# Performance work log

Measured on AMD Instinct MI355X. Metric: run time of the kernel, lower is better.

The kernel has to match this reference:

```python
import jax, jax.numpy as jnp
from jax import lax
import numpy as np

EPS = 1e-5
K = 3


def _conv(x, w, b, pad, dil=1, groups=1):
    out = lax.conv_general_dilated(
        x, w, (1, 1), [(pad, pad), (pad, pad)], rhs_dilation=(dil, dil),
        dimension_numbers=('NCHW', 'OIHW', 'NCHW'), feature_group_count=groups)
    return out + b[None, :, None, None]


def _bn(x, g, b, m, v):
    scale = g / jnp.sqrt(v + EPS)
    return (x - m[None, :, None, None]) * scale[None, :, None, None] + b[None, :, None, None]


def setup_inputs() -> dict:
    key = jax.random.key(0)
    ks = jax.random.split(key, 24)
    B, C, H, W = 8, 256, 48, 80
    Hd = 256  # hidden_channels
    n = lambda k, s, sc=0.05: (jax.random.normal(k, s, dtype=jnp.float32) * sc)
    return {
        'f_t_minus_2': jax.random.normal(ks[0], (B, C, H, W), dtype=jnp.float32),
        'f_t_minus_1': jax.random.normal(ks[1], (B, C, H, W), dtype=jnp.float32),
        'f_t':         jax.random.normal(ks[2], (B, C, H, W), dtype=jnp.float32),
        'ov_w1': n(ks[3], (Hd, 3 * C, 3, 3)), 'ov_b1': n(ks[4], (Hd,)),
        'bn1_g': jnp.ones((Hd,), jnp.float32), 'bn1_b': jnp.zeros((Hd,), jnp.float32),
        'bn1_m': n(ks[5], (Hd,)), 'bn1_v': jax.random.uniform(ks[6], (Hd,), jnp.float32, 0.5, 1.5),
        'ov_w2': n(ks[7], (Hd, Hd, 3, 3)), 'ov_b2': n(ks[8], (Hd,)),
        'bn2_g': jnp.ones((Hd,), jnp.float32), 'bn2_b': jnp.zeros((Hd,), jnp.float32),
        'bn2_m': n(ks[9], (Hd,)), 'bn2_v': jax.random.uniform(ks[10], (Hd,), jnp.float32, 0.5, 1.5),
        'g_w': n(ks[11], (C, Hd, 1, 1)), 'g_b': n(ks[12], (C,)),
        'fc1_w': n(ks[13], (512, 2 * C)), 'fc1_b': n(ks[14], (512,)),
        'fc2_w': n(ks[15], (C * K * K, 512)), 'fc2_b': n(ks[16], (C * K * K,)),
        'ap_w': n(ks[17], (1, 2 * C, 1, 1)), 'ap_b': n(ks[18], (1,)),
        'a_w': n(ks[19], (1, 2 * C, 1, 1)), 'a_b': jnp.ones((1,), jnp.float32),
    }


def reference(f_t_minus_2, f_t_minus_1, f_t,
              ov_w1, ov_b1, bn1_g, bn1_b, bn1_m, bn1_v,
              ov_w2, ov_b2, bn2_g, bn2_b, bn2_m, bn2_v,
              g_w, g_b, fc1_w, fc1_b, fc2_w, fc2_b,
              ap_w, ap_b, a_w, a_b):
    B, C, H, W = f_t.shape
    # (1) Overview-Net (GCM)
    f_concat = jnp.concatenate([f_t_minus_2, f_t_minus_1, f_t], axis=1)
    h = jax.nn.relu(_bn(_conv(f_concat, ov_w1, ov_b1, pad=2, dil=2), bn1_g, bn1_b, bn1_m, bn1_v))
    h = jax.nn.relu(_bn(_conv(h, ov_w2, ov_b2, pad=4, dil=4), bn2_g, bn2_b, bn2_m, bn2_v))
    g_pooled = h.mean(axis=(2, 3), keepdims=True)            # [B,Hd,1,1]
    G = _conv(g_pooled, g_w, g_b, pad=0)                     # [B,C,1,1]
    # (2) Focus-Net: FC-generated per-(batch,channel) 3x3 depthwise conv on (f_t, f_{t-1})
    Fs = jnp.concatenate([f_t, f_t_minus_1], axis=0)         # [2B,C,H,W]
    g_flat = jnp.repeat(G.reshape(B, C), 2, axis=0)          # [2B,C]
    gap = Fs.mean(axis=(2, 3))                               # [2B,C]
    fc_in = jnp.concatenate([g_flat, gap], axis=1)           # [2B,2C]
    w = jax.nn.silu(fc_in @ fc1_w.T + fc1_b) @ fc2_w.T + fc2_b  # [2B, C*9]
    w = w.reshape(2 * B * C, 1, K, K)
    x = Fs.reshape(1, 2 * B * C, H, W)
    out = lax.conv_general_dilated(
        x, w, (1, 1), [(1, 1), (1, 1)],
        dimension_numbers=('NCHW', 'OIHW', 'NCHW'), feature_group_count=2 * B * C)
    out = out.reshape(2 * B, C, H, W)
    f_t_mod, f_t1_mod = out[:B], out[B:]
    # (3) Dynamic fusion
    f_prev_cat = jnp.concatenate([f_t1_mod, f_t_minus_2], axis=1)
    alpha_prev = 0.3 + 0.4 * jax.nn.sigmoid(_conv(f_prev_cat, ap_w, ap_b, pad=0))
    f_prev = alpha_prev * f_t1_mod + (1.0 - alpha_prev) * f_t_minus_2
    f_cat = jnp.concatenate([f_t_mod, f_prev], axis=1)
    alpha = 0.6 + 0.3 * jax.nn.sigmoid(_conv(f_cat, a_w, a_b, pad=0))
    return alpha * f_t_mod + (1.0 - alpha) * f_prev
```

## Files before the change

kernel.cpp:

```cpp
#include <hip/hip_runtime.h>
#include <hip/hip_bf16.h>
#include <math.h>


typedef __bf16 bf16x8 __attribute__((ext_vector_type(8)));
typedef float f32x4 __attribute__((ext_vector_type(4)));
typedef __attribute__((address_space(1))) void as1_void;
typedef __attribute__((address_space(3))) void as3_void;

__global__ __launch_bounds__(256) void aux_kernel(
    const float* __restrict__ w1, const float* __restrict__ w2,
    const float* __restrict__ ob1, const float* __restrict__ g1, const float* __restrict__ b1,
    const float* __restrict__ m1, const float* __restrict__ v1,
    const float* __restrict__ ob2, const float* __restrict__ g2, const float* __restrict__ b2,
    const float* __restrict__ m2, const float* __restrict__ v2,
    __hip_bfloat16* __restrict__ wt1, __hip_bfloat16* __restrict__ wt2,
    __hip_bfloat16* __restrict__ h1p, float* __restrict__ gzero,
    float* __restrict__ cst)
{
  __shared__ float wl[1152];
  const int bid = blockIdx.x;
  const uint4 z4 = {0u, 0u, 0u, 0u};

  if (bid < 2048) {
    const float* w = (bid < 1536) ? w1 : w2;
    __hip_bfloat16* out = (bid < 1536) ? wt1 : wt2;
    const int IC = (bid < 1536) ? 768 : 256;
    const int lb = (bid < 1536) ? bid : (bid - 1536);
    const int nicb = IC >> 7;
    const int icb = lb % nicb, oc = lb / nicb;
    const int ic0 = icb * 128;
    const float* src = w + ((size_t)oc * IC + ic0) * 9;
    for (int k = threadIdx.x; k < 1152; k += 256) wl[k] = src[k];
    __syncthreads();
    if (threadIdx.x < 144) {
      const int tap = threadIdx.x / 16, ch = threadIdx.x % 16;
      union { __hip_bfloat16 h[8]; uint4 u; } pk;
#pragma unroll
      for (int j = 0; j < 8; j++) pk.h[j] = __float2bfloat16(wl[(ch * 8 + j) * 9 + tap]);
      *(uint4*)(out + ((size_t)tap * 256 + oc) * IC + ic0 + ch * 8) = pk.u;
    }
  } else if (bid < 3136) {
    const int s = (bid - 2048) * 256 + threadIdx.x;
    const int px = s >> 5, ch8 = s & 31;
    const int b = px / 1088, r = px % 1088;
    int y, x;
    if (r < 704) { const int yi = r / 88; y = (yi < 4) ? yi : 48 + yi; x = r % 88; }
    else { const int r2 = r - 704; y = 4 + (r2 >> 3); const int xi = r2 & 7; x = (xi < 4) ? xi : 80 + xi; }
    *(uint4*)(h1p + ((size_t)(b * 56 + y) * 88 + x) * 256 + ch8 * 8) = z4;
  } else if (bid < 3142) {
    ((uint4*)gzero)[(bid - 3136) * 256 + threadIdx.x] = z4;
  } else {
    const int i = threadIdx.x;
    float a1 = g1[i] / sqrtf(v1[i] + 1e-5f);
    cst[i]       = a1;
    cst[256 + i] = (ob1[i] - m1[i]) * a1 + b1[i];
    float a2 = g2[i] / sqrtf(v2[i] + 1e-5f);
    cst[512 + i] = a2;
    cst[768 + i] = (ob2[i] - m2[i]) * a2 + b2[i];
  }
}

__global__ __launch_bounds__(256) void pad_concat_kernel(
    const float* __restrict__ f2, const float* __restrict__ f1, const float* __restrict__ f0,
    __hip_bfloat16* __restrict__ out, float* __restrict__ gapv)
{
  int bid = blockIdx.x;
  const int cg = bid % 6; bid /= 6;
  const int y = bid % 48;
  const int b = bid / 48;

  __shared__ float tile[128 * 85];

  const float* src = (cg < 2) ? f2 : ((cg < 4) ? f1 : f0);
  const int ccbase = (cg & 1) * 128;
  const uint4 z4 = {0u, 0u, 0u, 0u};

#pragma unroll
  for (int it = 0; it < 10; it++) {
    const int idx = it * 256 + threadIdx.x;
    const int cl = idx / 20, x4 = idx % 20;
    const float4 v = *(const float4*)(src +
        (((size_t)b * 256 + ccbase + cl) * 48 + y) * 80 + x4 * 4);
    float* t = tile + cl * 85 + x4 * 4;
    t[0] = v.x; t[1] = v.y; t[2] = v.z; t[3] = v.w;
  }

  if (threadIdx.x < 32) {
    const int xb_ = threadIdx.x >> 3, ch8 = threadIdx.x & 7;
    const int xx = (xb_ < 2) ? xb_ : (80 + xb_);
    *(uint4*)(out + ((size_t)(b * 52 + y + 2) * 84 + xx) * 768 + cg * 128 + ch8 * 8) = z4;
  }
  if (y == 0 || y == 47) {
    const int r0 = (y == 0) ? 0 : 50;
    for (int idx = threadIdx.x; idx < 1344; idx += 256) {
      const int rr = idx / 672, rem = idx % 672;
      const int xx = rem >> 3, ch8 = rem & 7;
      *(uint4*)(out + ((size_t)(b * 52 + r0 + rr) * 84 + xx) * 768 + cg * 128 + ch8 * 8) = z4;
    }
  }
  __syncthreads();

  __hip_bfloat16* obase = out + ((size_t)(b * 52 + y + 2) * 84 + 2) * 768 + cg * 128;
#pragma unroll
  for (int it = 0; it < 5; it++) {
    const int idx = it * 256 + threadIdx.x;
    const int chunk = idx & 15, x = idx >> 4;
    const float* t = tile + chunk * 8 * 85 + x;
    union { __hip_bfloat16 h[8]; uint4 u; } pk;
#pragma unroll
    for (int j = 0; j < 8; j++) pk.h[j] = __float2bfloat16(t[j * 85]);
    *(uint4*)(obase + (size_t)x * 768 + chunk * 8) = pk.u;
  }

  if (cg >= 2) {
    const int i_gap = (cg >= 4) ? b : (b + 8);
    const int cl = threadIdx.x >> 1, half = threadIdx.x & 1;
    const float* t = tile + cl * 85 + half * 40;
    float s = 0.f;
#pragma unroll
    for (int k = 0; k < 40; k++) s += t[k];
    s += __shfl_xor(s, 1);
    if (half == 0) atomicAdd(&gapv[i_gap * 256 + ccbase + cl], s);
  }
}

template <int CIN, int HP, int WP, int DIL, int MODE>
__global__ __launch_bounds__(256) void conv_mfma_kernel(
    const __hip_bfloat16* __restrict__ inp, const __hip_bfloat16* __restrict__ wt,
    const float* __restrict__ bnA, const float* __restrict__ bnB,
    __hip_bfloat16* __restrict__ outp, float* __restrict__ gpool)
{
  __shared__ unsigned short As[8192] __attribute__((aligned(16)));
  __shared__ unsigned short Bs[8192] __attribute__((aligned(16)));

  int bid = blockIdx.x;
  bid = (bid & 7) * 60 + (bid >> 3);
  const int ocb = bid & 1; bid >>= 1;
  const int xb = bid % 5; bid /= 5;
  const int yb = bid % 6; bid /= 6;
  const int b = bid;
  const int y0 = yb * 8, x0 = xb * 16, oc0 = ocb * 128;

  const int t = threadIdx.x;
  const int w = t >> 6, l = t & 63;
  const int col16 = l & 15, quad = l >> 4;
  const int wm = w >> 1, wn = w & 1;
  const int rsub = l >> 3;
  const int jj = (l & 7) ^ rsub;

  f32x4 acc[4][4];
  const f32x4 zf = {0.f, 0.f, 0.f, 0.f};
#pragma unroll
  for (int i = 0; i < 4; i++)
#pragma unroll
    for (int j = 0; j < 4; j++) acc[i][j] = zf;

  for (int c0 = 0; c0 < CIN; c0 += 64) {
    for (int tap = 0; tap < 9; tap++) {
      const int ty = tap / 3, tx = tap - ty * 3;
      const __hip_bfloat16* inBase =
          inp + ((size_t)(b * HP + y0 + DIL * ty) * WP + (x0 + DIL * tx)) * CIN + jj * 8 + c0;
      const __hip_bfloat16* wBase = wt + (size_t)(tap * 256 + oc0) * CIN + jj * 8 + c0;
      __syncthreads();
#pragma unroll
      for (int i = 0; i < 4; i++) {
        const int q = i * 4 + w;
        const int m = q * 8 + rsub;
        const int ry = m >> 4, rx = m & 15;
        const __hip_bfloat16* gp = inBase + (ry * WP + rx) * CIN;
        __builtin_amdgcn_global_load_lds((as1_void*)gp,
            (as3_void*)((char*)As + q * 1024), 16, 0, 0);
      }
#pragma unroll
      for (int i = 0; i < 4; i++) {
        const int q = i * 4 + w;
        const int n = q * 8 + rsub;
        const __hip_bfloat16* gp = wBase + n * CIN;
        __builtin_amdgcn_global_load_lds((as1_void*)gp,
            (as3_void*)((char*)Bs + q * 1024), 16, 0, 0);
      }
      __syncthreads();
#pragma unroll
      for (int kiter = 0; kiter < 2; kiter++) {
        bf16x8 af[4], bg[4];
#pragma unroll
        for (int fi = 0; fi < 4; fi++) {
          const int m = wm * 64 + fi * 16 + col16;
          const int jc = (kiter * 4 + quad) ^ (m & 7);
          af[fi] = *(const bf16x8*)((const char*)As + m * 128 + jc * 16);
        }
#pragma unroll
        for (int fi = 0; fi < 4; fi++) {
          const int n = wn * 64 + fi * 16 + col16;
          const int jc = (kiter * 4 + quad) ^ (n & 7);
          bg[fi] = *(const bf16x8*)((const char*)Bs + n * 128 + jc * 16);
        }
#pragma unroll
        for (int fm_ = 0; fm_ < 4; fm_++)
#pragma unroll
          for (int fn_ = 0; fn_ < 4; fn_++)
            acc[fm_][fn_] = __builtin_amdgcn_mfma_f32_16x16x32_bf16(
                af[fm_], bg[fn_], acc[fm_][fn_], 0, 0, 0);
      }
    }
  }

  if (MODE == 0) {
#pragma unroll
    for (int fn_ = 0; fn_ < 4; fn_++) {
      const int oc = oc0 + wn * 64 + fn_ * 16 + col16;
      const float sa = bnA[oc], sb = bnB[oc];
#pragma unroll
      for (int fm_ = 0; fm_ < 4; fm_++) {
#pragma unroll
        for (int r = 0; r < 4; r++) {
          const int m = wm * 64 + fm_ * 16 + quad * 4 + r;
          const int y = y0 + (m >> 4), x = x0 + (m & 15);
          const float v = fmaxf(acc[fm_][fn_][r] * sa + sb, 0.f);
          outp[((size_t)(b * 56 + y + 4) * 88 + (x + 4)) * 256 + oc] = __float2bfloat16(v);
        }
      }
    }
  } else {
#pragma unroll
    for (int fn_ = 0; fn_ < 4; fn_++) {
      const int oc = oc0 + wn * 64 + fn_ * 16 + col16;
      const float sa = bnA[oc], sb = bnB[oc];
      float cs = 0.f;
#pragma unroll
      for (int fm_ = 0; fm_ < 4; fm_++)
#pragma unroll
        for (int r = 0; r < 4; r++)
          cs += fmaxf(acc[fm_][fn_][r] * sa + sb, 0.f);
      cs += __shfl_xor(cs, 16);
      cs += __shfl_xor(cs, 32);
      if (quad == 0) atomicAdd(&gpool[b * 256 + oc], cs);
    }
  }
}


__global__ __launch_bounds__(256) void fcG_kernel(
    const float* __restrict__ gpool, const float* __restrict__ gw,
    const float* __restrict__ gb, float* __restrict__ G)
{
  int b = blockIdx.x, oc = threadIdx.x;
  __shared__ float pool[256];
  pool[oc] = gpool[b * 256 + oc] * (1.f / 3840.f);
  __syncthreads();
  float s = gb[oc];
  const float* wr = gw + oc * 256;
  for (int c2 = 0; c2 < 256; c2++) s += pool[c2] * wr[c2];
  G[b * 256 + oc] = s;
}

__global__ __launch_bounds__(256) void fc1_kernel(
    const float* __restrict__ G, const float* __restrict__ gapv,
    const float* __restrict__ w, const float* __restrict__ bias,
    float* __restrict__ out1)
{
  __shared__ float fin[16][513];
  for (int idx = threadIdx.x; idx < 16 * 512; idx += 256) {
    int i = idx >> 9, k = idx & 511;
    fin[i][k] = (k < 256) ? G[(i >> 1) * 256 + k]
                          : gapv[i * 256 + (k - 256)] * (1.f / 3840.f);
  }
  __syncthreads();
  int g = blockIdx.x * 256 + threadIdx.x;
  int j = g >> 4, i = g & 15;
  float s = bias[j];
  const float* wr = w + j * 512;
  for (int k = 0; k < 512; k++) s += fin[i][k] * wr[k];
  out1[j * 16 + i] = s / (1.f + expf(-s));
}

__global__ __launch_bounds__(256) void fc2_kernel(
    const float* __restrict__ out1, const float* __restrict__ w,
    const float* __restrict__ bias, float* __restrict__ wdw)
{
  __shared__ float fin[16][513];
  for (int idx = threadIdx.x; idx < 16 * 512; idx += 256) {
    int i = idx >> 9, k = idx & 511;
    fin[i][k] = out1[k * 16 + i];
  }
  __syncthreads();
  int g = blockIdx.x * 256 + threadIdx.x;
  int j = g >> 4, i = g & 15;
  float s = bias[j];
  const float* wr = w + j * 512;
  for (int k = 0; k < 512; k++) s += fin[i][k] * wr[k];
  wdw[i * 2304 + j] = s;
}

__global__ __launch_bounds__(256) void dw_kernel(
    const float* __restrict__ f0, const float* __restrict__ f1,
    const float* __restrict__ wdw, float* __restrict__ fm)
{
  int i = blockIdx.x >> 8, c = blockIdx.x & 255;
  const float* src = (i < 8) ? (f0 + ((size_t)i * 256 + c) * 3840)
                             : (f1 + ((size_t)(i - 8) * 256 + c) * 3840);
  float* dst = fm + ((size_t)i * 256 + c) * 3840;
  __shared__ float w9s[9];
  __shared__ float tile[50][82];
  for (int k = threadIdx.x; k < 4100; k += 256) ((float*)tile)[k] = 0.f;
  if (threadIdx.x < 9) w9s[threadIdx.x] = wdw[i * 2304 + c * 9 + threadIdx.x];
  __syncthreads();
  for (int k = threadIdx.x; k < 960; k += 256) {
    const float4 v = *(const float4*)(src + k * 4);
    const int y = k / 20, xx = (k % 20) * 4;
    float* tp = &tile[y + 1][xx + 1];
    tp[0] = v.x; tp[1] = v.y; tp[2] = v.z; tp[3] = v.w;
  }
  __syncthreads();
  for (int k = threadIdx.x; k < 960; k += 256) {
    const int y = k / 20, xx = (k % 20) * 4;
    float r0 = 0.f, r1 = 0.f, r2 = 0.f, r3 = 0.f;
#pragma unroll
    for (int dy = 0; dy < 3; dy++) {
      const float* row = &tile[y + dy][xx];
      const float w0 = w9s[dy * 3], w1 = w9s[dy * 3 + 1], w2 = w9s[dy * 3 + 2];
      r0 += w0 * row[0] + w1 * row[1] + w2 * row[2];
      r1 += w0 * row[1] + w1 * row[2] + w2 * row[3];
      r2 += w0 * row[2] + w1 * row[3] + w2 * row[4];
      r3 += w0 * row[3] + w1 * row[4] + w2 * row[5];
    }
    float4 o; o.x = r0; o.y = r1; o.z = r2; o.w = r3;
    *(float4*)(dst + k * 4) = o;
  }
}

__global__ __launch_bounds__(640) void alpha_final_kernel(
    const float* __restrict__ fm, const float* __restrict__ f2,
    const float* __restrict__ apw, const float* __restrict__ apb,
    const float* __restrict__ aw, const float* __restrict__ ab,
    float* __restrict__ out)
{
  int b = blockIdx.x / 48, y = blockIdx.x % 48;
  int x = threadIdx.x % 80, g = threadIdx.x / 80;
  const float* ftm  = fm + ((size_t)(b * 256) + g * 32) * 3840 + y * 80 + x;
  const float* ft1m = fm + ((size_t)((b + 8) * 256) + g * 32) * 3840 + y * 80 + x;
  const float* ptm2 = f2 + ((size_t)(b * 256) + g * 32) * 3840 + y * 80 + x;

  float v0[32], v1[32], v2[32];
  float S = 0.f, T0 = 0.f, T1 = 0.f, T2 = 0.f;
#pragma unroll
  for (int cc = 0; cc < 32; cc++) {
    v0[cc] = ftm[(size_t)cc * 3840];
    v1[cc] = ft1m[(size_t)cc * 3840];
    v2[cc] = ptm2[(size_t)cc * 3840];
    const int c = g * 32 + cc;
    S  += apw[c] * v1[cc] + apw[256 + c] * v2[cc];
    T0 += aw[c] * v0[cc];
    T1 += aw[256 + c] * v1[cc];
    T2 += aw[256 + c] * v2[cc];
  }
  __shared__ float red[4][8][80];
  __shared__ float apl[80], alb[80];
  red[0][g][x] = S; red[1][g][x] = T0; red[2][g][x] = T1; red[3][g][x] = T2;
  __syncthreads();
  if (g == 0) {
    float s = 0.f, t0 = 0.f, t1 = 0.f, t2 = 0.f;
#pragma unroll
    for (int k = 0; k < 8; k++) {
      s += red[0][k][x]; t0 += red[1][k][x]; t1 += red[2][k][x]; t2 += red[3][k][x];
    }
    float ap = 0.3f + 0.4f / (1.f + expf(-(s + apb[0])));
    float A  = t0 + ap * t1 + (1.f - ap) * t2 + ab[0];
    float al = 0.6f + 0.3f / (1.f + expf(-A));
    apl[x] = ap; alb[x] = al;
  }
  __syncthreads();
  const float ap = apl[x], al = alb[x];
  float* ob = out + ((size_t)(b * 256) + g * 32) * 3840 + y * 80 + x;
#pragma unroll
  for (int cc = 0; cc < 32; cc++)
    ob[(size_t)cc * 3840] = al * v0[cc] + (1.f - al) * (ap * v1[cc] + (1.f - ap) * v2[cc]);
}


extern "C" void kernel_launch(void* const* d_in, const int* in_sizes, int n_in,
                              void* d_out, int out_size, void* d_ws, size_t ws_size,
                              hipStream_t stream)
{
  const float* f_tm2 = (const float*)d_in[0];
  const float* f_tm1 = (const float*)d_in[1];
  const float* f_t   = (const float*)d_in[2];
  const float* ov_w1 = (const float*)d_in[3];
  const float* ov_b1 = (const float*)d_in[4];
  const float* bn1_g = (const float*)d_in[5];
  const float* bn1_b = (const float*)d_in[6];
  const float* bn1_m = (const float*)d_in[7];
  const float* bn1_v = (const float*)d_in[8];
  const float* ov_w2 = (const float*)d_in[9];
  const float* ov_b2 = (const float*)d_in[10];
  const float* bn2_g = (const float*)d_in[11];
  const float* bn2_b = (const float*)d_in[12];
  const float* bn2_m = (const float*)d_in[13];
  const float* bn2_v = (const float*)d_in[14];
  const float* g_w   = (const float*)d_in[15];
  const float* g_b   = (const float*)d_in[16];
  const float* fc1_w = (const float*)d_in[17];
  const float* fc1_b = (const float*)d_in[18];
  const float* fc2_w = (const float*)d_in[19];
  const float* fc2_b = (const float*)d_in[20];
  const float* ap_w  = (const float*)d_in[21];
  const float* ap_b  = (const float*)d_in[22];
  const float* a_w   = (const float*)d_in[23];
  const float* a_b   = (const float*)d_in[24];

  char* ws = (char*)d_ws;
  float* fm            = (float*)ws;
  __hip_bfloat16* in1p = (__hip_bfloat16*)ws;
  __hip_bfloat16* wt1  = (__hip_bfloat16*)(ws + 53673984);
  __hip_bfloat16* wt2  = (__hip_bfloat16*)(ws + 57212928);
  __hip_bfloat16* h1p  = (__hip_bfloat16*)(ws + 58392576);
  float* gpool         = (float*)(ws + 78577664);
  float* gapv          = (float*)(ws + 78585856);
  float* Gv            = (float*)(ws + 78602240);
  float* out1          = (float*)(ws + 78610432);
  float* wdw           = (float*)(ws + 78643200);
  float* cst           = (float*)(ws + 79036416);

  aux_kernel<<<3143, 256, 0, stream>>>(ov_w1, ov_w2,
      ov_b1, bn1_g, bn1_b, bn1_m, bn1_v, ov_b2, bn2_g, bn2_b, bn2_m, bn2_v,
      wt1, wt2, h1p, gpool, cst);
  pad_concat_kernel<<<2304, 256, 0, stream>>>(f_tm2, f_tm1, f_t, in1p, gapv);

  conv_mfma_kernel<768, 52, 84, 2, 0><<<480, 256, 0, stream>>>(in1p, wt1, cst, cst + 256, h1p, nullptr);
  conv_mfma_kernel<256, 56, 88, 4, 1><<<480, 256, 0, stream>>>(h1p, wt2, cst + 512, cst + 768, nullptr, gpool);

  fcG_kernel<<<8, 256, 0, stream>>>(gpool, g_w, g_b, Gv);
  fc1_kernel<<<32, 256, 0, stream>>>(Gv, gapv, fc1_w, fc1_b, out1);
  fc2_kernel<<<144, 256, 0, stream>>>(out1, fc2_w, fc2_b, wdw);
  dw_kernel<<<4096, 256, 0, stream>>>(f_t, f_tm1, wdw, fm);
  alpha_final_kernel<<<384, 640, 0, stream>>>(fm, f_tm2, ap_w, ap_b, a_w, a_b, (float*)d_out);
}
```

Before: 444.6 us.

## Merge prep kernels, fold fcG into fc1, vectorize alpha-final with float4

Merges the pad/concat kernel and the auxiliary weight/pad/BN-constant kernel into a single prep launch, and zeroes gpool and gapv with one hipMemsetAsync instead of the zeroing blocks. The fcG matvec is folded into fc1, with each of the 32 blocks recomputing G redundantly so one launch and one global round-trip go away. The final alpha blend kernel now uses float4 loads and stores over 8 channels per thread, with a four-stage shared-memory reduction. The aim is to cut launch overhead and widen memory accesses, at the cost of repeated fcG work and more barriers in the reduction.

```diff
diff --git a/kernel.cpp b/kernel.cpp
--- a/kernel.cpp
+++ b/kernel.cpp
@@ -8,48 +8,112 @@
 typedef __attribute__((address_space(1))) void as1_void;
 typedef __attribute__((address_space(3))) void as3_void;
 
-__global__ __launch_bounds__(256) void aux_kernel(
+__device__ __forceinline__ void f4acc(float4& a, float s, const float4& v) {
+  a.x += s * v.x; a.y += s * v.y; a.z += s * v.z; a.w += s * v.w;
+}
+__device__ __forceinline__ float blend1(float al, float ap, float a, float b, float c) {
+  return al * a + (1.f - al) * (ap * b + (1.f - ap) * c);
+}
+
+__global__ __launch_bounds__(256) void prep_kernel(
+    const float* __restrict__ f2, const float* __restrict__ f1, const float* __restrict__ f0,
+    __hip_bfloat16* __restrict__ out, float* __restrict__ gapv,
     const float* __restrict__ w1, const float* __restrict__ w2,
     const float* __restrict__ ob1, const float* __restrict__ g1, const float* __restrict__ b1,
     const float* __restrict__ m1, const float* __restrict__ v1,
     const float* __restrict__ ob2, const float* __restrict__ g2, const float* __restrict__ b2,
     const float* __restrict__ m2, const float* __restrict__ v2,
     __hip_bfloat16* __restrict__ wt1, __hip_bfloat16* __restrict__ wt2,
-    __hip_bfloat16* __restrict__ h1p, float* __restrict__ gzero,
-    float* __restrict__ cst)
-{
-  __shared__ float wl[1152];
-  const int bid = blockIdx.x;
+    __hip_bfloat16* __restrict__ h1p, float* __restrict__ cst)
+{
+  __shared__ float shbuf[128 * 85];
   const uint4 z4 = {0u, 0u, 0u, 0u};
 
-  if (bid < 2048) {
-    const float* w = (bid < 1536) ? w1 : w2;
-    __hip_bfloat16* out = (bid < 1536) ? wt1 : wt2;
-    const int IC = (bid < 1536) ? 768 : 256;
-    const int lb = (bid < 1536) ? bid : (bid - 1536);
+  if (blockIdx.x < 2304) {
+    int bid = blockIdx.x;
+    const int cg = bid % 6; bid /= 6;
+    const int y = bid % 48;
+    const int b = bid / 48;
+    const float* src = (cg < 2) ? f2 : ((cg < 4) ? f1 : f0);
+    const int ccbase = (cg & 1) * 128;
+
+#pragma unroll
+    for (int it = 0; it < 10; it++) {
+      const int idx = it * 256 + threadIdx.x;
+      const int cl = idx / 20, x4 = idx % 20;
+      const float4 v = *(const float4*)(src +
+          (((size_t)b * 256 + ccbase + cl) * 48 + y) * 80 + x4 * 4);
+      float* t = shbuf + cl * 85 + x4 * 4;
+      t[0] = v.x; t[1] = v.y; t[2] = v.z; t[3] = v.w;
+    }
+
+    if (threadIdx.x < 32) {
+      const int xb_ = threadIdx.x >> 3, ch8 = threadIdx.x & 7;
+      const int xx = (xb_ < 2) ? xb_ : (80 + xb_);
+      *(uint4*)(out + ((size_t)(b * 52 + y + 2) * 84 + xx) * 768 + cg * 128 + ch8 * 8) = z4;
+    }
+    if (y == 0 || y == 47) {
+      const int r0 = (y == 0) ? 0 : 50;
+      for (int idx = threadIdx.x; idx < 1344; idx += 256) {
+        const int rr = idx / 672, rem = idx % 672;
+        const int xx = rem >> 3, ch8 = rem & 7;
+        *(uint4*)(out + ((size_t)(b * 52 + r0 + rr) * 84 + xx) * 768 + cg * 128 + ch8 * 8) = z4;
+      }
+    }
+    __syncthreads();
+
+    __hip_bfloat16* obase = out + ((size_t)(b * 52 + y + 2) * 84 + 2) * 768 + cg * 128;
+#pragma unroll
+    for (int it = 0; it < 5; it++) {
+      const int idx = it * 256 + threadIdx.x;
+      const int chunk = idx & 15, x = idx >> 4;
+      const float* t = shbuf + chunk * 8 * 85 + x;
+      union { __hip_bfloat16 h[8]; uint4 u; } pk;
+#pragma unroll
+      for (int j = 0; j < 8; j++) pk.h[j] = __float2bfloat16(t[j * 85]);
+      *(uint4*)(obase + (size_t)x * 768 + chunk * 8) = pk.u;
+    }
+
+    if (cg >= 2) {
+      const int i_gap = (cg >= 4) ? b : (b + 8);
+      const int cl = threadIdx.x >> 1, half = threadIdx.x & 1;
+      const float* t = shbuf + cl * 85 + half * 40;
+      float s = 0.f;
+#pragma unroll
+      for (int k = 0; k < 40; k++) s += t[k];
+      s += __shfl_xor(s, 1);
+      if (half == 0) atomicAdd(&gapv[i_gap * 256 + ccbase + cl], s);
+    }
+    return;
+  }
+
+  const int abid = blockIdx.x - 2304;
+  if (abid < 2048) {
+    const float* w = (abid < 1536) ? w1 : w2;
+    __hip_bfloat16* dst = (abid < 1536) ? wt1 : wt2;
+    const int IC = (abid < 1536) ? 768 : 256;
+    const int lb = (abid < 1536) ? abid : (abid - 1536);
     const int nicb = IC >> 7;
     const int icb = lb % nicb, oc = lb / nicb;
     const int ic0 = icb * 128;
     const float* src = w + ((size_t)oc * IC + ic0) * 9;
-    for (int k = threadIdx.x; k < 1152; k += 256) wl[k] = src[k];
+    for (int k = threadIdx.x; k < 1152; k += 256) shbuf[k] = src[k];
     __syncthreads();
     if (threadIdx.x < 144) {
       const int tap = threadIdx.x / 16, ch = threadIdx.x % 16;
       union { __hip_bfloat16 h[8]; uint4 u; } pk;
 #pragma unroll
-      for (int j = 0; j < 8; j++) pk.h[j] = __float2bfloat16(wl[(ch * 8 + j) * 9 + tap]);
-      *(uint4*)(out + ((size_t)tap * 256 + oc) * IC + ic0 + ch * 8) = pk.u;
-    }
-  } else if (bid < 3136) {
-    const int s = (bid - 2048) * 256 + threadIdx.x;
+      for (int j = 0; j < 8; j++) pk.h[j] = __float2bfloat16(shbuf[(ch * 8 + j) * 9 + tap]);
+      *(uint4*)(dst + ((size_t)tap * 256 + oc) * IC + ic0 + ch * 8) = pk.u;
+    }
+  } else if (abid < 3136) {
+    const int s = (abid - 2048) * 256 + threadIdx.x;
     const int px = s >> 5, ch8 = s & 31;
     const int b = px / 1088, r = px % 1088;
     int y, x;
     if (r < 704) { const int yi = r / 88; y = (yi < 4) ? yi : 48 + yi; x = r % 88; }
     else { const int r2 = r - 704; y = 4 + (r2 >> 3); const int xi = r2 & 7; x = (xi < 4) ? xi : 80 + xi; }
     *(uint4*)(h1p + ((size_t)(b * 56 + y) * 88 + x) * 256 + ch8 * 8) = z4;
-  } else if (bid < 3142) {
-    ((uint4*)gzero)[(bid - 3136) * 256 + threadIdx.x] = z4;
   } else {
     const int i = threadIdx.x;
     float a1 = g1[i] / sqrtf(v1[i] + 1e-5f);
@@ -61,70 +125,6 @@
   }
 }
 
-__global__ __launch_bounds__(256) void pad_concat_kernel(
-    const float* __restrict__ f2, const float* __restrict__ f1, const float* __restrict__ f0,
-    __hip_bfloat16* __restrict__ out, float* __restrict__ gapv)
-{
-  int bid = blockIdx.x;
-  const int cg = bid % 6; bid /= 6;
-  const int y = bid % 48;
-  const int b = bid / 48;
-
-  __shared__ float tile[128 * 85];
-
-  const float* src = (cg < 2) ? f2 : ((cg < 4) ? f1 : f0);
-  const int ccbase = (cg & 1) * 128;
-  const uint4 z4 = {0u, 0u, 0u, 0u};
-
-#pragma unroll
-  for (int it = 0; it < 10; it++) {
-    const int idx = it * 256 + threadIdx.x;
-    const int cl = idx / 20, x4 = idx % 20;
-    const float4 v = *(const float4*)(src +
-        (((size_t)b * 256 + ccbase + cl) * 48 + y) * 80 + x4 * 4);
-    float* t = tile + cl * 85 + x4 * 4;
-    t[0] = v.x; t[1] = v.y; t[2] = v.z; t[3] = v.w;
-  }
-
-  if (threadIdx.x < 32) {
-    const int xb_ = threadIdx.x >> 3, ch8 = threadIdx.x & 7;
-    const int xx = (xb_ < 2) ? xb_ : (80 + xb_);
-    *(uint4*)(out + ((size_t)(b * 52 + y + 2) * 84 + xx) * 768 + cg * 128 + ch8 * 8) = z4;
-  }
-  if (y == 0 || y == 47) {
-    const int r0 = (y == 0) ? 0 : 50;
-    for (int idx = threadIdx.x; idx < 1344; idx += 256) {
-      const int rr = idx / 672, rem = idx % 672;
-      const int xx = rem >> 3, ch8 = rem & 7;
-      *(uint4*)(out + ((size_t)(b * 52 + r0 + rr) * 84 + xx) * 768 + cg * 128 + ch8 * 8) = z4;
-    }
-  }
-  __syncthreads();
-
-  __hip_bfloat16* obase = out + ((size_t)(b * 52 + y + 2) * 84 + 2) * 768 + cg * 128;
-#pragma unroll
-  for (int it = 0; it < 5; it++) {
-    const int idx = it * 256 + threadIdx.x;
-    const int chunk = idx & 15, x = idx >> 4;
-    const float* t = tile + chunk * 8 * 85 + x;
-    union { __hip_bfloat16 h[8]; uint4 u; } pk;
-#pragma unroll
-    for (int j = 0; j < 8; j++) pk.h[j] = __float2bfloat16(t[j * 85]);
-    *(uint4*)(obase + (size_t)x * 768 + chunk * 8) = pk.u;
-  }
-
-  if (cg >= 2) {
-    const int i_gap = (cg >= 4) ? b : (b + 8);
-    const int cl = threadIdx.x >> 1, half = threadIdx.x & 1;
-    const float* t = tile + cl * 85 + half * 40;
-    float s = 0.f;
-#pragma unroll
-    for (int k = 0; k < 40; k++) s += t[k];
-    s += __shfl_xor(s, 1);
-    if (half == 0) atomicAdd(&gapv[i_gap * 256 + ccbase + cl], s);
-  }
-}
-
 template <int CIN, int HP, int WP, int DIL, int MODE>
 __global__ __launch_bounds__(256) void conv_mfma_kernel(
     const __hip_bfloat16* __restrict__ inp, const __hip_bfloat16* __restrict__ wt,
@@ -241,29 +241,38 @@
 }
 
 
-__global__ __launch_bounds__(256) void fcG_kernel(
+__global__ __launch_bounds__(256) void fc1_kernel(
     const float* __restrict__ gpool, const float* __restrict__ gw,
-    const float* __restrict__ gb, float* __restrict__ G)
-{
-  int b = blockIdx.x, oc = threadIdx.x;
-  __shared__ float pool[256];
-  pool[oc] = gpool[b * 256 + oc] * (1.f / 3840.f);
-  __syncthreads();
-  float s = gb[oc];
-  const float* wr = gw + oc * 256;
-  for (int c2 = 0; c2 < 256; c2++) s += pool[c2] * wr[c2];
-  G[b * 256 + oc] = s;
-}
-
-__global__ __launch_bounds__(256) void fc1_kernel(
-    const float* __restrict__ G, const float* __restrict__ gapv,
+    const float* __restrict__ gb, const float* __restrict__ gapv,
     const float* __restrict__ w, const float* __restrict__ bias,
     float* __restrict__ out1)
 {
+  __shared__ float pool[8][256];
+  __shared__ float Gl[8][256];
   __shared__ float fin[16][513];
+  for (int idx = threadIdx.x; idx < 2048; idx += 256)
+    pool[idx >> 8][idx & 255] = gpool[idx] * (1.f / 3840.f);
+  __syncthreads();
+  {
+    const int oc = threadIdx.x;
+    float s0, s1, s2, s3, s4, s5, s6, s7;
+    const float g0 = gb[oc];
+    s0 = s1 = s2 = s3 = s4 = s5 = s6 = s7 = g0;
+    const float* wr = gw + oc * 256;
+    for (int c = 0; c < 256; c++) {
+      const float wv = wr[c];
+      s0 += pool[0][c] * wv; s1 += pool[1][c] * wv;
+      s2 += pool[2][c] * wv; s3 += pool[3][c] * wv;
+      s4 += pool[4][c] * wv; s5 += pool[5][c] * wv;
+      s6 += pool[6][c] * wv; s7 += pool[7][c] * wv;
+    }
+    Gl[0][oc] = s0; Gl[1][oc] = s1; Gl[2][oc] = s2; Gl[3][oc] = s3;
+    Gl[4][oc] = s4; Gl[5][oc] = s5; Gl[6][oc] = s6; Gl[7][oc] = s7;
+  }
+  __syncthreads();
   for (int idx = threadIdx.x; idx < 16 * 512; idx += 256) {
     int i = idx >> 9, k = idx & 511;
-    fin[i][k] = (k < 256) ? G[(i >> 1) * 256 + k]
+    fin[i][k] = (k < 256) ? Gl[i >> 1][k]
                           : gapv[i * 256 + (k - 256)] * (1.f / 3840.f);
   }
   __syncthreads();
@@ -336,46 +345,94 @@
     const float* __restrict__ aw, const float* __restrict__ ab,
     float* __restrict__ out)
 {
-  int b = blockIdx.x / 48, y = blockIdx.x % 48;
-  int x = threadIdx.x % 80, g = threadIdx.x / 80;
-  const float* ftm  = fm + ((size_t)(b * 256) + g * 32) * 3840 + y * 80 + x;
-  const float* ft1m = fm + ((size_t)((b + 8) * 256) + g * 32) * 3840 + y * 80 + x;
-  const float* ptm2 = f2 + ((size_t)(b * 256) + g * 32) * 3840 + y * 80 + x;
-
-  float v0[32], v1[32], v2[32];
-  float S = 0.f, T0 = 0.f, T1 = 0.f, T2 = 0.f;
-#pragma unroll
-  for (int cc = 0; cc < 32; cc++) {
-    v0[cc] = ftm[(size_t)cc * 3840];
-    v1[cc] = ft1m[(size_t)cc * 3840];
-    v2[cc] = ptm2[(size_t)cc * 3840];
-    const int c = g * 32 + cc;
-    S  += apw[c] * v1[cc] + apw[256 + c] * v2[cc];
-    T0 += aw[c] * v0[cc];
-    T1 += aw[256 + c] * v1[cc];
-    T2 += aw[256 + c] * v2[cc];
-  }
-  __shared__ float red[4][8][80];
-  __shared__ float apl[80], alb[80];
-  red[0][g][x] = S; red[1][g][x] = T0; red[2][g][x] = T1; red[3][g][x] = T2;
-  __syncthreads();
-  if (g == 0) {
-    float s = 0.f, t0 = 0.f, t1 = 0.f, t2 = 0.f;
-#pragma unroll
-    for (int k = 0; k < 8; k++) {
-      s += red[0][k][x]; t0 += red[1][k][x]; t1 += red[2][k][x]; t2 += red[3][k][x];
-    }
-    float ap = 0.3f + 0.4f / (1.f + expf(-(s + apb[0])));
-    float A  = t0 + ap * t1 + (1.f - ap) * t2 + ab[0];
-    float al = 0.6f + 0.3f / (1.f + expf(-A));
-    apl[x] = ap; alb[x] = al;
-  }
-  __syncthreads();
-  const float ap = apl[x], al = alb[x];
-  float* ob = out + ((size_t)(b * 256) + g * 32) * 3840 + y * 80 + x;
-#pragma unroll
-  for (int cc = 0; cc < 32; cc++)
-    ob[(size_t)cc * 3840] = al * v0[cc] + (1.f - al) * (ap * v1[cc] + (1.f - ap) * v2[cc]);
+  const int b = blockIdx.x / 48, y = blockIdx.x % 48;
+  const int x4 = threadIdx.x % 20, g = threadIdx.x / 20;
+  const size_t base = (size_t)(b * 256 + g * 8) * 3840 + y * 80 + x4 * 4;
+  const float* ftm  = fm + base;
+  const float* ft1m = fm + (size_t)2048 * 3840 + base;
+  const float* ptm2 = f2 + base;
+
+  float4 v0[8], v1[8], v2[8];
+  float4 S  = {0.f, 0.f, 0.f, 0.f}, T0 = {0.f, 0.f, 0.f, 0.f};
+  float4 T1 = {0.f, 0.f, 0.f, 0.f}, T2 = {0.f, 0.f, 0.f, 0.f};
+#pragma unroll
+  for (int cc = 0; cc < 8; cc++) {
+    v0[cc] = *(const float4*)(ftm  + (size_t)cc * 3840);
+    v1[cc] = *(const float4*)(ft1m + (size_t)cc * 3840);
+    v2[cc] = *(const float4*)(ptm2 + (size_t)cc * 3840);
+    const int c = g * 8 + cc;
+    const float wa1 = apw[c], wa2 = apw[256 + c];
+    const float wb0 = aw[c],  wb1 = aw[256 + c];
+    f4acc(S, wa1, v1[cc]);  f4acc(S, wa2, v2[cc]);
+    f4acc(T0, wb0, v0[cc]);
+    f4acc(T1, wb1, v1[cc]);
+    f4acc(T2, wb1, v2[cc]);
+  }
+
+  __shared__ float4 red[32][21];
+  __shared__ float4 apl4[20], all4[20];
+  float4 St, T0t, T1t, T2t;
+
+  red[g][x4] = S;  __syncthreads();
+  if (threadIdx.x < 20) {
+    float4 a = red[0][threadIdx.x];
+    for (int k = 1; k < 32; k++) { const float4 r = red[k][threadIdx.x];
+      a.x += r.x; a.y += r.y; a.z += r.z; a.w += r.w; }
+    St = a;
+  }
+  __syncthreads();
+  red[g][x4] = T0; __syncthreads();
+  if (threadIdx.x < 20) {
+    float4 a = red[0][threadIdx.x];
+    for (int k = 1; k < 32; k++) { const float4 r = red[k][threadIdx.x];
+      a.x += r.x; a.y += r.y; a.z += r.z; a.w += r.w; }
+    T0t = a;
+  }
+  __syncthreads();
+  red[g][x4] = T1; __syncthreads();
+  if (threadIdx.x < 20) {
+    float4 a = red[0][threadIdx.x];
+    for (int k = 1; k < 32; k++) { const float4 r = red[k][threadIdx.x];
+      a.x += r.x; a.y += r.y; a.z += r.z; a.w += r.w; }
+    T1t = a;
+  }
+  __syncthreads();
+  red[g][x4] = T2; __syncthreads();
+  if (threadIdx.x < 20) {
+    float4 a = red[0][threadIdx.x];
+    for (int k = 1; k < 32; k++) { const float4 r = red[k][threadIdx.x];
+      a.x += r.x; a.y += r.y; a.z += r.z; a.w += r.w; }
+    T2t = a;
+
+    const float apb0 = apb[0], ab0 = ab[0];
+    float4 ap, al;
+    ap.x = 0.3f + 0.4f / (1.f + expf(-(St.x + apb0)));
+    ap.y = 0.3f + 0.4f / (1.f + expf(-(St.y + apb0)));
+    ap.z = 0.3f + 0.4f / (1.f + expf(-(St.z + apb0)));
+    ap.w = 0.3f + 0.4f / (1.f + expf(-(St.w + apb0)));
+    const float Ax = T0t.x + ap.x * T1t.x + (1.f - ap.x) * T2t.x + ab0;
+    const float Ay = T0t.y + ap.y * T1t.y + (1.f - ap.y) * T2t.y + ab0;
+    const float Az = T0t.z + ap.z * T1t.z + (1.f - ap.z) * T2t.z + ab0;
+    const float Aw = T0t.w + ap.w * T1t.w + (1.f - ap.w) * T2t.w + ab0;
+    al.x = 0.6f + 0.3f / (1.f + expf(-Ax));
+    al.y = 0.6f + 0.3f / (1.f + expf(-Ay));
+    al.z = 0.6f + 0.3f / (1.f + expf(-Az));
+    al.w = 0.6f + 0.3f / (1.f + expf(-Aw));
+    apl4[threadIdx.x] = ap; all4[threadIdx.x] = al;
+  }
+  __syncthreads();
+
+  const float4 ap = apl4[x4], al = all4[x4];
+  float* ob = out + base;
+#pragma unroll
+  for (int cc = 0; cc < 8; cc++) {
+    float4 r;
+    r.x = blend1(al.x, ap.x, v0[cc].x, v1[cc].x, v2[cc].x);
+    r.y = blend1(al.y, ap.y, v0[cc].y, v1[cc].y, v2[cc].y);
+    r.z = blend1(al.z, ap.z, v0[cc].z, v1[cc].z, v2[cc].z);
+    r.w = blend1(al.w, ap.w, v0[cc].w, v1[cc].w, v2[cc].w);
+    *(float4*)(ob + (size_t)cc * 3840) = r;
+  }
 }
 
 
@@ -417,21 +474,20 @@
   __hip_bfloat16* h1p  = (__hip_bfloat16*)(ws + 58392576);
   float* gpool         = (float*)(ws + 78577664);
   float* gapv          = (float*)(ws + 78585856);
-  float* Gv            = (float*)(ws + 78602240);
   float* out1          = (float*)(ws + 78610432);
   float* wdw           = (float*)(ws + 78643200);
   float* cst           = (float*)(ws + 79036416);
 
-  aux_kernel<<<3143, 256, 0, stream>>>(ov_w1, ov_w2,
-      ov_b1, bn1_g, bn1_b, bn1_m, bn1_v, ov_b2, bn2_g, bn2_b, bn2_m, bn2_v,
-      wt1, wt2, h1p, gpool, cst);
-  pad_concat_kernel<<<2304, 256, 0, stream>>>(f_tm2, f_tm1, f_t, in1p, gapv);
+  hipMemsetAsync(gpool, 0, 24576, stream);
+
+  prep_kernel<<<5441, 256, 0, stream>>>(f_tm2, f_tm1, f_t, in1p, gapv,
+      ov_w1, ov_w2, ov_b1, bn1_g, bn1_b, bn1_m, bn1_v,
+      ov_b2, bn2_g, bn2_b, bn2_m, bn2_v, wt1, wt2, h1p, cst);
 
   conv_mfma_kernel<768, 52, 84, 2, 0><<<480, 256, 0, stream>>>(in1p, wt1, cst, cst + 256, h1p, nullptr);
   conv_mfma_kernel<256, 56, 88, 4, 1><<<480, 256, 0, stream>>>(h1p, wt2, cst + 512, cst + 768, nullptr, gpool);
 
-  fcG_kernel<<<8, 256, 0, stream>>>(gpool, g_w, g_b, Gv);
-  fc1_kernel<<<32, 256, 0, stream>>>(Gv, gapv, fc1_w, fc1_b, out1);
+  fc1_kernel<<<32, 256, 0, stream>>>(gpool, g_w, g_b, gapv, fc1_w, fc1_b, out1);
   fc2_kernel<<<144, 256, 0, stream>>>(out1, fc2_w, fc2_b, wdw);
   dw_kernel<<<4096, 256, 0, stream>>>(f_t, f_tm1, wdw, fm);
   alpha_final_kernel<<<384, 640, 0, stream>>>(fm, f_tm2, ap_w, ap_b, a_w, a_b, (float*)d_out);
```

Result: no change. 448.4 us (+0.9%).
